# Performance work log

Hardware: AMD Instinct MI355X
Metric: run time of the kernel (lower is better)

Reference implementation:

```python
import jax, jax.numpy as jnp
import numpy as np
from jax import lax

MAX_LENGTH = 64
BATCH = 65536


def setup_inputs() -> dict:
    key = jax.random.key(0)
    ks = jax.random.split(key, 14)
    init = lambda k, shape, fan_in: jax.random.uniform(k, shape, jnp.float32, -1.0, 1.0) / np.sqrt(fan_in)
    return {
        "a": jax.random.randint(ks[0], (BATCH, MAX_LENGTH), 0, 10, dtype=jnp.int64) if jax.config.jax_enable_x64 else jax.random.randint(ks[0], (BATCH, MAX_LENGTH), 0, 10, dtype=jnp.int32),
        "b": jax.random.randint(ks[1], (BATCH, MAX_LENGTH), 0, 10, dtype=jnp.int32),
        "Ea": jax.random.normal(ks[2], (10, 8), jnp.float32),
        "Eb": jax.random.normal(ks[3], (10, 8), jnp.float32),
        "W1": init(ks[4], (64, 18), 18), "b1": init(ks[5], (64,), 18),
        "W2": init(ks[6], (32, 64), 64), "b2": init(ks[7], (32,), 64),
        "Wd": init(ks[8], (10, 32), 32), "bd": init(ks[9], (10,), 32),
        "Wc": init(ks[10], (2, 32), 32), "bc": init(ks[11], (2,), 32),
    }


def reference(a, b, Ea, Eb, W1, b1, W2, b2, Wd, bd, Wc, bc):
    # a, b: [B, L] int digits in [0,10)
    B, L = a.shape
    a_emb = Ea[a]  # [B, L, 8]
    b_emb = Eb[b]  # [B, L, 8]

    def step(carry_in, x):
        ae, be = x  # each [B, 8]
        combined = jnp.concatenate([ae, be, carry_in], axis=1)  # [B, 18]
        h = jax.nn.relu(combined @ W1.T + b1)  # [B, 64]
        h = jax.nn.relu(h @ W2.T + b2)         # [B, 32]
        digit_logit = h @ Wd.T + bd            # [B, 10]
        carry_logit = h @ Wc.T + bc            # [B, 2]
        return jax.nn.softmax(carry_logit, axis=1), (digit_logit, carry_logit)

    carry0 = jnp.zeros((B, 2), dtype=a_emb.dtype).at[:, 0].set(1.0)
    xs = (jnp.swapaxes(a_emb, 0, 1), jnp.swapaxes(b_emb, 0, 1))  # [L, B, 8]
    _, (digit_logits, carry_logits) = lax.scan(step, carry0, xs)
    # [L, B, *] -> [B, L, *]
    return jnp.swapaxes(digit_logits, 0, 1), jnp.swapaxes(carry_logits, 0, 1)
```

## Files before the change

kernel.cpp:

```cpp
#include <hip/hip_runtime.h>
#include <hip/hip_bf16.h>
#include <stdint.h>

#define NBATCH 65536
#define LSEQ   64

typedef __attribute__((ext_vector_type(8))) _Float16 half8;
typedef __attribute__((ext_vector_type(2))) __fp16  fp16x2;
typedef __attribute__((ext_vector_type(4))) float f32x4;
typedef __attribute__((ext_vector_type(4), aligned(8))) float f32x4u;
typedef __attribute__((ext_vector_type(4))) int   i32x4;

static __device__ __forceinline__ int relu_pk_f16(float x, float y){
    union { fp16x2 h; int i; } u;
    u.h = __builtin_amdgcn_cvt_pkrtz(fmaxf(x, 0.f), fmaxf(y, 0.f));
    return u.i;
}

__global__ __launch_bounds__(256, 4)
void mlp_mfma_kernel(const int* __restrict__ a, const int* __restrict__ b,
                     const float* __restrict__ Ea, const float* __restrict__ Eb,
                     const float* __restrict__ W1, const float* __restrict__ b1,
                     const float* __restrict__ W2, const float* __restrict__ b2,
                     const float* __restrict__ Wd, const float* __restrict__ bd,
                     const float* __restrict__ Wc, const float* __restrict__ bc,
                     float* __restrict__ out)
{
    __shared__ __attribute__((aligned(16))) _Float16 Pab[100*72];
    __shared__ unsigned char pkL[64*64];
    __shared__ int scr[4][16*17 + 16];

    const int tid = threadIdx.x;
    const int wv  = tid >> 6;
    const int l   = tid & 63;
    const int q   = l >> 4;
    const int n   = l & 15;

    const int sBase = blockIdx.x * 64;

    {
        const i32x4* ap = (const i32x4*)(a + (size_t)sBase * LSEQ);
        const i32x4* bp = (const i32x4*)(b + (size_t)sBase * LSEQ);
        #pragma unroll
        for (int k = 0; k < 4; k++){
            int v = tid + k*256;
            i32x4 av = ap[v], bv = bp[v];
            int ns = v >> 4, s0 = (v & 15) << 2;
            pkL[(s0+0)*64 + ns] = (unsigned char)(av[0]*10 + bv[0]);
            pkL[(s0+1)*64 + ns] = (unsigned char)(av[1]*10 + bv[1]);
            pkL[(s0+2)*64 + ns] = (unsigned char)(av[2]*10 + bv[2]);
            pkL[(s0+3)*64 + ns] = (unsigned char)(av[3]*10 + bv[3]);
        }
    }

    for (int e = tid; e < 6400; e += 256){
        int p = e >> 6, j = e & 63;
        int da = p / 10, db = p - da*10;
        float acc = b1[j] + W1[j*18 + 17];
        #pragma unroll
        for (int k2 = 0; k2 < 8; k2++){
            acc = fmaf(Ea[da*8 + k2], W1[j*18 + k2],     acc);
            acc = fmaf(Eb[db*8 + k2], W1[j*18 + 8 + k2], acc);
        }
        Pab[p*72 + j] = (_Float16)acc;
    }

    half8 dcr[2];
    #pragma unroll
    for (int kc = 0; kc < 2; kc++){
        union { half8 v; _Float16 e[8]; } ud;
        #pragma unroll
        for (int jj = 0; jj < 8; jj++){
            int j = kc*32 + q*8 + jj;
            ud.e[jj] = (_Float16)(W1[j*18 + 16] - W1[j*18 + 17]);
        }
        dcr[kc] = ud.v;
    }

    half8 w2f[2][2];
    #pragma unroll
    for (int mt = 0; mt < 2; mt++)
        #pragma unroll
        for (int kc = 0; kc < 2; kc++){
            union { half8 v; _Float16 e[8]; } uw;
            int m = mt*16 + n;
            #pragma unroll
            for (int jj = 0; jj < 8; jj++)
                uw.e[jj] = (_Float16)W2[m*64 + kc*32 + q*8 + jj];
            w2f[mt][kc] = uw.v;
        }

    half8 w3f;
    {
        union { half8 v; _Float16 e[8]; } u3;
        #pragma unroll
        for (int jj = 0; jj < 8; jj++){
            int k = q*8 + jj;
            float x = 0.f;
            if (n < 10)      x = Wd[n*32+k];
            else if (n < 12) x = Wc[(n-10)*32+k];
            u3.e[jj] = (_Float16)x;
        }
        w3f = u3.v;
    }

    f32x4 bias2a = { b2[q*4+0], b2[q*4+1], b2[q*4+2], b2[q*4+3] };
    f32x4 bias2b = { b2[16+q*4+0], b2[16+q*4+1], b2[16+q*4+2], b2[16+q*4+3] };
    f32x4 bias3;
    #pragma unroll
    for (int r = 0; r < 4; r++){
        int m = q*4 + r;
        bias3[r] = (m < 10) ? bd[m] : (m < 12 ? bc[m-10] : 0.f);
    }

    __syncthreads();

    const int tn = sBase + wv*16 + n;
    const int lc = wv*16 + n;
    int* scrw = scr[wv];
    char* outc = (char*)out;
    const unsigned dbase = (unsigned)tn*2560u + (unsigned)q*16u;
    const unsigned cbase = (unsigned)(NBATCH*(size_t)LSEQ*10*4) + (unsigned)tn*512u;
    const int bpa = (32 + n) << 2;

    float carry = 1.0f;
    int idxN;
    half8 PA[2][2];
    {
        int i0 = pkL[lc];
        const _Float16* r0 = &Pab[i0*72 + q*8];
        PA[0][0] = *(const half8*)r0;
        PA[0][1] = *(const half8*)(r0 + 32);
        idxN = pkL[64 + lc];
    }

    for (int so = 0; so < LSEQ; so += 8){
        f32x4 stg[8];
        #pragma unroll
        for (int u = 0; u < 8; u++){
            const int s = so + u;
            const int cur = u & 1, nxt = cur ^ 1;

            _Float16 ch = (_Float16)carry;
            half8 c8 = {ch,ch,ch,ch,ch,ch,ch,ch};
            half8 z  = {};
            half8 h10 = __builtin_elementwise_max(PA[cur][0] + c8*dcr[0], z);
            half8 h11 = __builtin_elementwise_max(PA[cur][1] + c8*dcr[1], z);

            {
                const _Float16* rn = &Pab[idxN*72 + q*8];
                PA[nxt][0] = *(const half8*)rn;
                PA[nxt][1] = *(const half8*)(rn + 32);
            }
            int idxN2 = pkL[(((s+2)&63)<<6) + lc];

            f32x4 acc2a = bias2a, acc2b = bias2b;
            acc2a = __builtin_amdgcn_mfma_f32_16x16x32_f16(w2f[0][0], h10, acc2a, 0,0,0);
            acc2a = __builtin_amdgcn_mfma_f32_16x16x32_f16(w2f[0][1], h11, acc2a, 0,0,0);
            acc2b = __builtin_amdgcn_mfma_f32_16x16x32_f16(w2f[1][0], h10, acc2b, 0,0,0);
            acc2b = __builtin_amdgcn_mfma_f32_16x16x32_f16(w2f[1][1], h11, acc2b, 0,0,0);

            scrw[(2*q+0)*17 + n]   = relu_pk_f16(acc2a[0], acc2a[1]);
            scrw[(2*q+1)*17 + n]   = relu_pk_f16(acc2a[2], acc2a[3]);
            scrw[(8+2*q+0)*17 + n] = relu_pk_f16(acc2b[0], acc2b[1]);
            scrw[(8+2*q+1)*17 + n] = relu_pk_f16(acc2b[2], acc2b[3]);
            __builtin_amdgcn_wave_barrier();
            int d0 = scrw[(q*4+0)*17 + n];
            int d1 = scrw[(q*4+1)*17 + n];
            int d2 = scrw[(q*4+2)*17 + n];
            int d3 = scrw[(q*4+3)*17 + n];
            __builtin_amdgcn_wave_barrier();
            union { i32x4 d; half8 v; } uh2;
            uh2.d = i32x4{d0, d1, d2, d3};

            f32x4 acc3 = bias3;
            acc3 = __builtin_amdgcn_mfma_f32_16x16x32_f16(w3f, uh2.v, acc3, 0,0,0);

            float diff = acc3[2] - acc3[3];
            int dv = __builtin_amdgcn_ds_bpermute(bpa, __float_as_int(diff));
            carry = 1.0f / (1.0f + __expf(-__int_as_float(dv)));

            stg[u] = acc3;
            idxN = idxN2;
        }

        const unsigned dbq = dbase + (unsigned)so*40u;
        const unsigned cbq = cbase + (unsigned)so*8u;
        if (q < 2){
            #pragma unroll
            for (int u = 0; u < 8; u++)
                *(f32x4u*)(outc + dbq + u*40) = stg[u];
        } else if (q == 2){
            #pragma unroll
            for (int u = 0; u < 8; u++){
                *(float2*)(outc + dbq + u*40) = float2{stg[u][0], stg[u][1]};
                *(float2*)(outc + cbq + u*8)  = float2{stg[u][2], stg[u][3]};
            }
        }
    }
}

extern "C" void kernel_launch(void* const* d_in, const int* in_sizes, int n_in,
                              void* d_out, int out_size, void* d_ws, size_t ws_size,
                              hipStream_t stream) {
    const int*   a  = (const int*)d_in[0];
    const int*   b  = (const int*)d_in[1];
    const float* Ea = (const float*)d_in[2];
    const float* Eb = (const float*)d_in[3];
    const float* W1 = (const float*)d_in[4];
    const float* b1 = (const float*)d_in[5];
    const float* W2 = (const float*)d_in[6];
    const float* b2 = (const float*)d_in[7];
    const float* Wd = (const float*)d_in[8];
    const float* bd = (const float*)d_in[9];
    const float* Wc = (const float*)d_in[10];
    const float* bc = (const float*)d_in[11];

    mlp_mfma_kernel<<<NBATCH / 64, 256, 0, stream>>>(a, b, Ea, Eb, W1, b1,
                                                     W2, b2, Wd, bd, Wc, bc,
                                                     (float*)d_out);
}
```

Baseline: 288.2 us.

## Permute W2 rows to drop LDS transpose, pack digit indices per sample

W2 rows are permuted and the layer-2 biases remapped so that the MFMA output lanes already hold the K-layout the third MFMA needs as B operand. This removes the per-step LDS scratch write/read round trip and its two wave barriers. Input digit pairs are also stored packed, four per word, in a per-sample row-major LDS array. Each wave then loads 8 steps of indices with one int2 read instead of one byte load per step. The dependent chain per step gets shorter, at the cost of some extra shift and mask work for index extraction.

```diff
diff --git a/kernel.cpp b/kernel.cpp
--- a/kernel.cpp
+++ b/kernel.cpp
@@ -27,8 +27,7 @@
                      float* __restrict__ out)
 {
     __shared__ __attribute__((aligned(16))) _Float16 Pab[100*72];
-    __shared__ unsigned char pkL[64*64];
-    __shared__ int scr[4][16*17 + 16];
+    __shared__ __attribute__((aligned(8))) unsigned char pkT[64*72];
 
     const int tid = threadIdx.x;
     const int wv  = tid >> 6;
@@ -46,10 +45,11 @@
             int v = tid + k*256;
             i32x4 av = ap[v], bv = bp[v];
             int ns = v >> 4, s0 = (v & 15) << 2;
-            pkL[(s0+0)*64 + ns] = (unsigned char)(av[0]*10 + bv[0]);
-            pkL[(s0+1)*64 + ns] = (unsigned char)(av[1]*10 + bv[1]);
-            pkL[(s0+2)*64 + ns] = (unsigned char)(av[2]*10 + bv[2]);
-            pkL[(s0+3)*64 + ns] = (unsigned char)(av[3]*10 + bv[3]);
+            unsigned pk = (unsigned)(av[0]*10 + bv[0])
+                        | ((unsigned)(av[1]*10 + bv[1]) << 8)
+                        | ((unsigned)(av[2]*10 + bv[2]) << 16)
+                        | ((unsigned)(av[3]*10 + bv[3]) << 24);
+            *(unsigned*)&pkT[ns*72 + s0] = pk;
         }
     }
 
@@ -79,16 +79,17 @@
 
     half8 w2f[2][2];
     #pragma unroll
-    for (int mt = 0; mt < 2; mt++)
+    for (int mt = 0; mt < 2; mt++){
+        const int row = ((n >> 2) << 3) + (mt << 2) + (n & 3);
         #pragma unroll
         for (int kc = 0; kc < 2; kc++){
             union { half8 v; _Float16 e[8]; } uw;
-            int m = mt*16 + n;
             #pragma unroll
             for (int jj = 0; jj < 8; jj++)
-                uw.e[jj] = (_Float16)W2[m*64 + kc*32 + q*8 + jj];
+                uw.e[jj] = (_Float16)W2[row*64 + kc*32 + q*8 + jj];
             w2f[mt][kc] = uw.v;
         }
+    }
 
     half8 w3f;
     {
@@ -104,8 +105,8 @@
         w3f = u3.v;
     }
 
-    f32x4 bias2a = { b2[q*4+0], b2[q*4+1], b2[q*4+2], b2[q*4+3] };
-    f32x4 bias2b = { b2[16+q*4+0], b2[16+q*4+1], b2[16+q*4+2], b2[16+q*4+3] };
+    f32x4 bias2a = { b2[8*q+0], b2[8*q+1], b2[8*q+2], b2[8*q+3] };
+    f32x4 bias2b = { b2[8*q+4], b2[8*q+5], b2[8*q+6], b2[8*q+7] };
     f32x4 bias3;
     #pragma unroll
     for (int r = 0; r < 4; r++){
@@ -117,28 +118,29 @@
 
     const int tn = sBase + wv*16 + n;
     const int lc = wv*16 + n;
-    int* scrw = scr[wv];
     char* outc = (char*)out;
     const unsigned dbase = (unsigned)tn*2560u + (unsigned)q*16u;
     const unsigned cbase = (unsigned)(NBATCH*(size_t)LSEQ*10*4) + (unsigned)tn*512u;
     const int bpa = (32 + n) << 2;
 
     float carry = 1.0f;
-    int idxN;
+    int c0, c1;
     half8 PA[2][2];
     {
-        int i0 = pkL[lc];
+        int2 cc = *(const int2*)&pkT[lc*72];
+        c0 = cc.x; c1 = cc.y;
+        int i0 = c0 & 255;
         const _Float16* r0 = &Pab[i0*72 + q*8];
         PA[0][0] = *(const half8*)r0;
         PA[0][1] = *(const half8*)(r0 + 32);
-        idxN = pkL[64 + lc];
     }
 
     for (int so = 0; so < LSEQ; so += 8){
+        int2 nd = *(const int2*)&pkT[lc*72 + (so < 56 ? so + 8 : so)];
+
         f32x4 stg[8];
         #pragma unroll
         for (int u = 0; u < 8; u++){
-            const int s = so + u;
             const int cur = u & 1, nxt = cur ^ 1;
 
             _Float16 ch = (_Float16)carry;
@@ -148,11 +150,14 @@
             half8 h11 = __builtin_elementwise_max(PA[cur][1] + c8*dcr[1], z);
 
             {
-                const _Float16* rn = &Pab[idxN*72 + q*8];
+                int ib;
+                if (u < 3)       ib = (c0 >> (8*(u+1))) & 255;
+                else if (u < 7)  ib = (c1 >> (8*(u-3))) & 255;
+                else             ib = nd.x & 255;
+                const _Float16* rn = &Pab[ib*72 + q*8];
                 PA[nxt][0] = *(const half8*)rn;
                 PA[nxt][1] = *(const half8*)(rn + 32);
             }
-            int idxN2 = pkL[(((s+2)&63)<<6) + lc];
 
             f32x4 acc2a = bias2a, acc2b = bias2b;
             acc2a = __builtin_amdgcn_mfma_f32_16x16x32_f16(w2f[0][0], h10, acc2a, 0,0,0);
@@ -160,18 +165,11 @@
             acc2b = __builtin_amdgcn_mfma_f32_16x16x32_f16(w2f[1][0], h10, acc2b, 0,0,0);
             acc2b = __builtin_amdgcn_mfma_f32_16x16x32_f16(w2f[1][1], h11, acc2b, 0,0,0);
 
-            scrw[(2*q+0)*17 + n]   = relu_pk_f16(acc2a[0], acc2a[1]);
-            scrw[(2*q+1)*17 + n]   = relu_pk_f16(acc2a[2], acc2a[3]);
-            scrw[(8+2*q+0)*17 + n] = relu_pk_f16(acc2b[0], acc2b[1]);
-            scrw[(8+2*q+1)*17 + n] = relu_pk_f16(acc2b[2], acc2b[3]);
-            __builtin_amdgcn_wave_barrier();
-            int d0 = scrw[(q*4+0)*17 + n];
-            int d1 = scrw[(q*4+1)*17 + n];
-            int d2 = scrw[(q*4+2)*17 + n];
-            int d3 = scrw[(q*4+3)*17 + n];
-            __builtin_amdgcn_wave_barrier();
             union { i32x4 d; half8 v; } uh2;
-            uh2.d = i32x4{d0, d1, d2, d3};
+            uh2.d = i32x4{ relu_pk_f16(acc2a[0], acc2a[1]),
+                           relu_pk_f16(acc2a[2], acc2a[3]),
+                           relu_pk_f16(acc2b[0], acc2b[1]),
+                           relu_pk_f16(acc2b[2], acc2b[3]) };
 
             f32x4 acc3 = bias3;
             acc3 = __builtin_amdgcn_mfma_f32_16x16x32_f16(w3f, uh2.v, acc3, 0,0,0);
@@ -181,7 +179,6 @@
             carry = 1.0f / (1.0f + __expf(-__int_as_float(dv)));
 
             stg[u] = acc3;
-            idxN = idxN2;
         }
 
         const unsigned dbq = dbase + (unsigned)so*40u;
@@ -197,6 +194,7 @@
                 *(float2*)(outc + cbq + u*8)  = float2{stg[u][2], stg[u][3]};
             }
         }
+        c0 = nd.x; c1 = nd.y;
     }
 }
 
```

After: 286.4 us. About the same (-0.6%).
